# Optimization experiments

Measured on AMD Instinct MI355X. Metric: run time of the kernel, lower is better.

Reference implementation:

```python
import jax, jax.numpy as jnp
import numpy as np

N = 8192   # instances in bag
L = 384    # feature dim (dino_bloom_small -> self.L = 384)
D = 128    # attention hidden dim (self.D)
C = 5      # class_count


def setup_inputs() -> dict:
    key = jax.random.key(0)
    ks = jax.random.split(key, 9)
    s = 0.05
    return {
        "x": jax.random.normal(ks[0], (N, L), dtype=jnp.float32),
        # attention_multi_column: Linear(L,D) -> Tanh -> Linear(D,C)
        "aW1": jax.random.normal(ks[1], (L, D), dtype=jnp.float32) * s,
        "ab1": jax.random.normal(ks[2], (D,), dtype=jnp.float32) * s,
        "aW2": jax.random.normal(ks[3], (D, C), dtype=jnp.float32) * s,
        "ab2": jax.random.normal(ks[4], (C,), dtype=jnp.float32) * s,
        # per-class classifiers: Linear(L,64) -> ReLU -> Linear(64,1), batched over C
        "cW1": jax.random.normal(ks[5], (C, L, 64), dtype=jnp.float32) * s,
        "cb1": jax.random.normal(ks[6], (C, 64), dtype=jnp.float32) * s,
        "cW2": jax.random.normal(ks[7], (C, 64), dtype=jnp.float32) * s,
        "cb2": jax.random.normal(ks[8], (C,), dtype=jnp.float32) * s,
    }


def _pairwise_euclidean(ft):
    # ||a-b|| via Gram expansion; avoids the O(N^2*L) broadcast intermediate
    sq = jnp.sum(ft * ft, axis=1)                      # [N]
    d2 = sq[:, None] + sq[None, :] - 2.0 * (ft @ ft.T)  # [N,N]
    d2 = jnp.maximum(d2, 0.0)
    # safe sqrt (zero on diagonal, matches torch.norm subgradient convention)
    return jnp.where(d2 > 0.0, jnp.sqrt(jnp.where(d2 > 0.0, d2, 1.0)), 0.0)


def reference(x, aW1, ab1, aW2, ab2, cW1, cb1, cW2, cb2):
    ft = x  # encoder is identity for dino_bloom_small
    dist = _pairwise_euclidean(ft)                      # [N,N]
    # multicolumn attention: logits per class, softmax over instances
    att = jnp.tanh(ft @ aW1 + ab1) @ aW2 + ab2          # [N,C]
    att_sm = jax.nn.softmax(att, axis=0)                # softmax over N per class
    bag = att_sm.T @ ft                                 # [C,L] bag features per class
    # per-class classifier heads, batched over class dim
    h = jax.nn.relu(jnp.einsum('cl,clh->ch', bag, cW1) + cb1)  # [C,64]
    pred = jnp.sum(h * cW2, axis=1) + cb2               # [C]
    return pred[None, :], dist
```

## Files before the change

kernel.cpp:

```cpp
#include <hip/hip_runtime.h>
#include <cstdint>
#include <cstddef>

#define N_INST 8192
#define L_DIM  384
#define D_DIM  128
#define C_CLS  5

typedef __bf16 bf16x8 __attribute__((ext_vector_type(8)));
typedef float  f32x4  __attribute__((ext_vector_type(4)));
typedef float  f32x4u __attribute__((ext_vector_type(4), aligned(4)));

typedef __attribute__((address_space(1))) void gvoid_t;
typedef __attribute__((address_space(3))) void lvoid_t;

__device__ __forceinline__ unsigned short f2bf(float f) {
  unsigned u = __float_as_uint(f);
  unsigned r = (u + 0x7FFFu + ((u >> 16) & 1u)) >> 16;
  return (unsigned short)r;
}
__device__ __forceinline__ float bf2f(unsigned short b) {
  return __uint_as_float(((unsigned)b) << 16);
}

__device__ __forceinline__ void gload_lds16(const void* g, void* lds) {
  __builtin_amdgcn_global_load_lds(
      (gvoid_t*)(uintptr_t)g,
      (lvoid_t*)(uint32_t)(uintptr_t)lds,
      16, 0, 0);
}

__global__ __launch_bounds__(256) void prep_x_kernel(
    const float* __restrict__ x, unsigned short* __restrict__ xbf,
    float* __restrict__ sq) {
  int w = threadIdx.x >> 6, lane = threadIdx.x & 63;
  int row = blockIdx.x * 4 + w;
  const float* xr = x + (size_t)row * L_DIM;
  unsigned short* br = xbf + (size_t)row * L_DIM;
  float s = 0.f;
#pragma unroll
  for (int k = 0; k < 6; ++k) {
    float v = xr[lane + 64 * k];
    unsigned short b = f2bf(v);
    br[lane + 64 * k] = b;
    float vb = bf2f(b);
    s = fmaf(vb, vb, s);
  }
#pragma unroll
  for (int off = 32; off; off >>= 1) s += __shfl_down(s, off, 64);
  if (lane == 0) sq[row] = s;
}

__global__ __launch_bounds__(256) void prep_w_kernel(
    const float* __restrict__ aW1, unsigned short* __restrict__ w1t) {
  int idx = blockIdx.x * 256 + threadIdx.x;
  int d = idx / L_DIM, l = idx - d * L_DIM;
  w1t[idx] = f2bf(aW1[(size_t)l * D_DIM + d]);
}

__global__ __launch_bounds__(256, 2) void attn_gemm_kernel(
    const unsigned short* __restrict__ amat,
    const unsigned short* __restrict__ bmat,
    const float* __restrict__ bias,
    const float* __restrict__ aW2,
    const float* __restrict__ ab2,
    float* __restrict__ exp_att,
    float* __restrict__ colsum) {
  __shared__ alignas(16) unsigned short As[128][64];
  __shared__ alignas(16) unsigned short Bs[128][64];
  __shared__ float aW2_l[D_DIM * C_CLS];
  __shared__ float part[128][8][C_CLS];
  __shared__ float cs_l[C_CLS];

  int tid = threadIdx.x;
  int w = tid >> 6, lane = tid & 63;
  int wr = w >> 1, wc = w & 1;
  int i0 = blockIdx.x * 128;

  for (int idx = tid; idx < D_DIM * C_CLS; idx += 256) aW2_l[idx] = aW2[idx];
  if (tid < C_CLS) cs_l[tid] = 0.f;

  const unsigned short* asrc = amat + (size_t)i0 * L_DIM;
  const unsigned short* bsrc = bmat;

  f32x4 acc[4][4];
#pragma unroll
  for (int m = 0; m < 4; ++m)
#pragma unroll
    for (int n = 0; n < 4; ++n) acc[m][n] = (f32x4){0.f, 0.f, 0.f, 0.f};

  int lrow = lane & 15, lkb = lane >> 4;

  for (int kc = 0; kc < 6; ++kc) {
    int k0 = kc * 64;
#pragma unroll
    for (int c = 0; c < 4; ++c) {
      int rb = c * 32 + w * 8;
      gload_lds16(asrc + (size_t)(rb + (lane >> 3)) * L_DIM + k0 + (lane & 7) * 8,
                  &As[rb][0]);
      gload_lds16(bsrc + (size_t)(rb + (lane >> 3)) * L_DIM + k0 + (lane & 7) * 8,
                  &Bs[rb][0]);
    }
    __syncthreads();
#pragma unroll
    for (int kk = 0; kk < 64; kk += 32) {
      bf16x8 af[4], bfr[4];
#pragma unroll
      for (int m = 0; m < 4; ++m)
        af[m] = *(const bf16x8*)&As[wr * 64 + m * 16 + lrow][kk + lkb * 8];
#pragma unroll
      for (int n = 0; n < 4; ++n)
        bfr[n] = *(const bf16x8*)&Bs[wc * 64 + n * 16 + lrow][kk + lkb * 8];
#pragma unroll
      for (int m = 0; m < 4; ++m)
#pragma unroll
        for (int n = 0; n < 4; ++n)
          acc[m][n] = __builtin_amdgcn_mfma_f32_16x16x32_bf16(
              bfr[n], af[m], acc[m][n], 0, 0, 0);
    }
    __syncthreads();
  }

  int q = wc * 4 + lkb;
#pragma unroll
  for (int m = 0; m < 4; ++m) {
    int row_l = wr * 64 + m * 16 + lrow;
    float p[C_CLS] = {0.f, 0.f, 0.f, 0.f, 0.f};
#pragma unroll
    for (int n = 0; n < 4; ++n) {
      int d0 = wc * 64 + n * 16 + lkb * 4;
#pragma unroll
      for (int r = 0; r < 4; ++r) {
        float v = tanhf(acc[m][n][r] + bias[d0 + r]);
        const float* wrow = &aW2_l[(d0 + r) * C_CLS];
#pragma unroll
        for (int c = 0; c < C_CLS; ++c) p[c] = fmaf(v, wrow[c], p[c]);
      }
    }
#pragma unroll
    for (int c = 0; c < C_CLS; ++c) part[row_l][q][c] = p[c];
  }
  __syncthreads();

  if (tid < 128) {
    int gi = i0 + tid;
    float a[C_CLS];
#pragma unroll
    for (int c = 0; c < C_CLS; ++c) a[c] = ab2[c];
#pragma unroll
    for (int qq = 0; qq < 8; ++qq)
#pragma unroll
      for (int c = 0; c < C_CLS; ++c) a[c] += part[tid][qq][c];
#pragma unroll
    for (int c = 0; c < C_CLS; ++c) {
      float e = expf(a[c]);
      exp_att[(size_t)gi * C_CLS + c] = e;
      atomicAdd(&cs_l[c], e);
    }
  }
  __syncthreads();
  if (tid < C_CLS) atomicAdd(&colsum[tid], cs_l[tid]);
}

__global__ __launch_bounds__(256) void head_kernel(
    const unsigned short* __restrict__ xbf, const float* __restrict__ sqv,
    float* __restrict__ F) {
  int w = threadIdx.x >> 6, lane = threadIdx.x & 63;
  int i = blockIdx.x * 4 + w;
  float a0 = 0.f, a1 = 0.f, a2 = 0.f;
  if (lane < 48) {
    const unsigned short* xi = xbf + (size_t)i * L_DIM + lane * 8;
    const unsigned short* x0 = xbf + lane * 8;
    const unsigned short* x1 = xbf + L_DIM + lane * 8;
    const unsigned short* x2 = xbf + 2 * L_DIM + lane * 8;
#pragma unroll
    for (int e = 0; e < 8; ++e) {
      float v = bf2f(xi[e]);
      a0 = fmaf(v, bf2f(x0[e]), a0);
      a1 = fmaf(v, bf2f(x1[e]), a1);
      a2 = fmaf(v, bf2f(x2[e]), a2);
    }
  }
#pragma unroll
  for (int off = 32; off; off >>= 1) {
    a0 += __shfl_down(a0, off, 64);
    a1 += __shfl_down(a1, off, 64);
    a2 += __shfl_down(a2, off, 64);
  }
  if (lane == 0) {
    float si = sqv[i];
    float dots[3] = {a0, a1, a2};
#pragma unroll
    for (int j = 0; j < 3; ++j) {
      float d2 = si + sqv[j] - 2.f * dots[j];
      float dv = (d2 > 0.f) ? sqrtf(d2) : 0.f;
      if (i == j) dv = 0.f;
      F[5 + (size_t)i * N_INST + j] = dv;
    }
  }
}

__global__ __launch_bounds__(256, 2) void dist_kernel(
    const unsigned short* __restrict__ xbf, const float* __restrict__ sqv,
    float* __restrict__ F) {
  __shared__ alignas(16) unsigned short As[128][64];
  __shared__ alignas(16) unsigned short Bs[128][64];

  int tid = threadIdx.x;
  int w = tid >> 6, lane = tid & 63;
  int wr = w >> 1, wc = w & 1;

  int b = blockIdx.x;
  int ti = (int)((129.0 - sqrt(129.0 * 129.0 - 8.0 * (double)b)) * 0.5);
  while ((ti + 1) * (129 - (ti + 1)) / 2 <= b) ++ti;
  while (ti * (129 - ti) / 2 > b) --ti;
  int tj = ti + (b - ti * (129 - ti) / 2);
  int i0 = ti * 128, j0 = tj * 128;

  const unsigned short* asrc = xbf + (size_t)i0 * L_DIM;
  const unsigned short* bsrc = xbf + (size_t)j0 * L_DIM;

  f32x4 acc[4][4];
#pragma unroll
  for (int m = 0; m < 4; ++m)
#pragma unroll
    for (int n = 0; n < 4; ++n) acc[m][n] = (f32x4){0.f, 0.f, 0.f, 0.f};

  int lrow = lane & 15, lkb = lane >> 4;
  int schunk = ((lane & 7) ^ (lane >> 3)) * 8;
  int swz = (lane & 7) << 3;

  for (int kc = 0; kc < 6; ++kc) {
    int k0 = kc * 64;
#pragma unroll
    for (int c = 0; c < 4; ++c) {
      int rb = c * 32 + w * 8;
      gload_lds16(asrc + (size_t)(rb + (lane >> 3)) * L_DIM + k0 + schunk,
                  &As[rb][0]);
      gload_lds16(bsrc + (size_t)(rb + (lane >> 3)) * L_DIM + k0 + schunk,
                  &Bs[rb][0]);
    }
    __syncthreads();
#pragma unroll
    for (int kk = 0; kk < 64; kk += 32) {
      bf16x8 af[4], bfr[4];
#pragma unroll
      for (int m = 0; m < 4; ++m)
        af[m] = *(const bf16x8*)&As[wr * 64 + m * 16 + lrow][(kk + lkb * 8) ^ swz];
#pragma unroll
      for (int n = 0; n < 4; ++n)
        bfr[n] = *(const bf16x8*)&Bs[wc * 64 + n * 16 + lrow][(kk + lkb * 8) ^ swz];
#pragma unroll
      for (int m = 0; m < 4; ++m)
#pragma unroll
        for (int n = 0; n < 4; ++n)
          acc[m][n] = __builtin_amdgcn_mfma_f32_16x16x32_bf16(
              bfr[n], af[m], acc[m][n], 0, 0, 0);
    }
    __syncthreads();
  }

  bool mirror = (ti != tj);
#pragma unroll
  for (int m = 0; m < 4; ++m) {
    int gi = i0 + wr * 64 + m * 16 + lrow;
    float si = sqv[gi];
    float* orow = F + 5 + (size_t)gi * N_INST;
#pragma unroll
    for (int n = 0; n < 4; ++n) {
      int gjb = j0 + wc * 64 + n * 16 + lkb * 4;
      f32x4 sj = *(const f32x4*)&sqv[gjb];
      f32x4u o;
#pragma unroll
      for (int r = 0; r < 4; ++r) {
        float d2 = si + sj[r] - 2.f * acc[m][n][r];
        float dv = (d2 > 0.f) ? sqrtf(d2) : 0.f;
        if (gi == gjb + r) dv = 0.f;
        o[r] = dv;
      }
      *(f32x4u*)&orow[gjb] = o;
      if (mirror) {
#pragma unroll
        for (int r = 0; r < 4; ++r)
          F[5 + (size_t)(gjb + r) * N_INST + gi] = o[r];
      }
    }
  }
}

__global__ __launch_bounds__(256) void bag_kernel(
    const float* __restrict__ x, const float* __restrict__ exp_att,
    float* __restrict__ bagU) {
  int t = threadIdx.x;
  int rbase = blockIdx.x * 32;
  float acc0[C_CLS] = {0, 0, 0, 0, 0}, acc1[C_CLS] = {0, 0, 0, 0, 0};
  int l0 = t, l1 = t + 256;
  for (int i = rbase; i < rbase + 32; ++i) {
    const float* xr = x + (size_t)i * L_DIM;
    float e[C_CLS];
#pragma unroll
    for (int c = 0; c < C_CLS; ++c) e[c] = exp_att[(size_t)i * C_CLS + c];
    float x0 = xr[l0];
#pragma unroll
    for (int c = 0; c < C_CLS; ++c) acc0[c] = fmaf(e[c], x0, acc0[c]);
    if (t < 128) {
      float x1 = xr[l1];
#pragma unroll
      for (int c = 0; c < C_CLS; ++c) acc1[c] = fmaf(e[c], x1, acc1[c]);
    }
  }
#pragma unroll
  for (int c = 0; c < C_CLS; ++c) atomicAdd(&bagU[c * L_DIM + l0], acc0[c]);
  if (t < 128)
#pragma unroll
    for (int c = 0; c < C_CLS; ++c) atomicAdd(&bagU[c * L_DIM + l1], acc1[c]);
}

__global__ __launch_bounds__(256) void final_kernel(
    const float* __restrict__ bagU, const float* __restrict__ colsum,
    const float* __restrict__ cW1, const float* __restrict__ cb1,
    const float* __restrict__ cW2, const float* __restrict__ cb2,
    float* __restrict__ out) {
  __shared__ float bag_s[C_CLS * L_DIM];
  __shared__ float h_s[C_CLS * 64];
  int t = threadIdx.x;
  for (int idx = t; idx < C_CLS * L_DIM; idx += 256) {
    int c = idx / L_DIM;
    bag_s[idx] = bagU[idx] / colsum[c];
  }
  __syncthreads();
  for (int idx = t; idx < C_CLS * 64; idx += 256) {
    int c = idx >> 6, hh = idx & 63;
    float acc = cb1[idx];
    for (int l = 0; l < L_DIM; ++l)
      acc = fmaf(bag_s[c * L_DIM + l], cW1[(size_t)(c * L_DIM + l) * 64 + hh], acc);
    h_s[idx] = fmaxf(acc, 0.f) * cW2[idx];
  }
  __syncthreads();
  if (t < C_CLS) {
    float p = cb2[t];
    for (int hh = 0; hh < 64; ++hh) p += h_s[t * 64 + hh];
    out[t] = p;
  }
}

extern "C" void kernel_launch(void* const* d_in, const int* in_sizes, int n_in,
                              void* d_out, int out_size, void* d_ws,
                              size_t ws_size, hipStream_t stream) {
  const float* x   = (const float*)d_in[0];
  const float* aW1 = (const float*)d_in[1];
  const float* ab1 = (const float*)d_in[2];
  const float* aW2 = (const float*)d_in[3];
  const float* ab2 = (const float*)d_in[4];
  const float* cW1 = (const float*)d_in[5];
  const float* cb1 = (const float*)d_in[6];
  const float* cW2 = (const float*)d_in[7];
  const float* cb2 = (const float*)d_in[8];
  float* outp = (float*)d_out;

  char* ws = (char*)d_ws;
  unsigned short* xbf = (unsigned short*)(ws);
  unsigned short* w1t = (unsigned short*)(ws + 6291456);
  float* sq           = (float*)(ws + 6389760);
  float* exp_att      = (float*)(ws + 6422528);
  float* colsum       = (float*)(ws + 6586368);
  float* bagU         = (float*)(ws + 6586432);

  hipMemsetAsync(ws + 6586368, 0, 64 + C_CLS * L_DIM * 4, stream);

  prep_x_kernel<<<2048, 256, 0, stream>>>(x, xbf, sq);
  prep_w_kernel<<<192, 256, 0, stream>>>(aW1, w1t);
  attn_gemm_kernel<<<64, 256, 0, stream>>>(xbf, w1t, ab1, aW2, ab2, exp_att,
                                           colsum);
  bag_kernel<<<256, 256, 0, stream>>>(x, exp_att, bagU);
  final_kernel<<<1, 256, 0, stream>>>(bagU, colsum, cW1, cb1, cW2, cb2, outp);
  head_kernel<<<2048, 256, 0, stream>>>(xbf, sq, outp);
  dist_kernel<<<2080, 256, 0, stream>>>(xbf, sq, outp);
}
```

Baseline: 210.2 us.

## Compute full distance matrix with aligned column offset instead of symmetric mirroring

The distance kernel stops computing only upper-triangle tiles and mirroring them with scattered transposed stores. It now computes all 64x64 tiles, with columns shifted by 27 so that row stores land on 16-byte aligned addresses given the 5-float output offset. The head kernel is rewritten as an MFMA tile that fills the first 27 columns of every row. This removes strided uncoalesced mirror writes at the cost of roughly doubling the GEMM work.

After: 186.7 us. 11.2% less time.

```diff
diff --git a/kernel.cpp b/kernel.cpp
--- a/kernel.cpp
+++ b/kernel.cpp
@@ -165,37 +165,52 @@
 __global__ __launch_bounds__(256) void head_kernel(
     const unsigned short* __restrict__ xbf, const float* __restrict__ sqv,
     float* __restrict__ F) {
-  int w = threadIdx.x >> 6, lane = threadIdx.x & 63;
-  int i = blockIdx.x * 4 + w;
-  float a0 = 0.f, a1 = 0.f, a2 = 0.f;
-  if (lane < 48) {
-    const unsigned short* xi = xbf + (size_t)i * L_DIM + lane * 8;
-    const unsigned short* x0 = xbf + lane * 8;
-    const unsigned short* x1 = xbf + L_DIM + lane * 8;
-    const unsigned short* x2 = xbf + 2 * L_DIM + lane * 8;
-#pragma unroll
-    for (int e = 0; e < 8; ++e) {
-      float v = bf2f(xi[e]);
-      a0 = fmaf(v, bf2f(x0[e]), a0);
-      a1 = fmaf(v, bf2f(x1[e]), a1);
-      a2 = fmaf(v, bf2f(x2[e]), a2);
-    }
-  }
-#pragma unroll
-  for (int off = 32; off; off >>= 1) {
-    a0 += __shfl_down(a0, off, 64);
-    a1 += __shfl_down(a1, off, 64);
-    a2 += __shfl_down(a2, off, 64);
-  }
-  if (lane == 0) {
-    float si = sqv[i];
-    float dots[3] = {a0, a1, a2};
-#pragma unroll
-    for (int j = 0; j < 3; ++j) {
-      float d2 = si + sqv[j] - 2.f * dots[j];
-      float dv = (d2 > 0.f) ? sqrtf(d2) : 0.f;
-      if (i == j) dv = 0.f;
-      F[5 + (size_t)i * N_INST + j] = dv;
+  int tid = threadIdx.x;
+  int w = tid >> 6, lane = tid & 63;
+  int lrow = lane & 15, lkb = lane >> 4;
+  int rowb = blockIdx.x * 128 + w * 32;
+
+  f32x4 acc[2][2];
+#pragma unroll
+  for (int m = 0; m < 2; ++m)
+#pragma unroll
+    for (int n = 0; n < 2; ++n) acc[m][n] = (f32x4){0.f, 0.f, 0.f, 0.f};
+
+  for (int t = 0; t < 12; ++t) {
+    bf16x8 af[2], bfr[2];
+#pragma unroll
+    for (int m = 0; m < 2; ++m)
+      af[m] = *(const bf16x8*)(xbf + (size_t)(rowb + m * 16 + lrow) * L_DIM +
+                               t * 32 + lkb * 8);
+#pragma unroll
+    for (int n = 0; n < 2; ++n)
+      bfr[n] = *(const bf16x8*)(xbf + (size_t)(n * 16 + lrow) * L_DIM +
+                                t * 32 + lkb * 8);
+#pragma unroll
+    for (int m = 0; m < 2; ++m)
+#pragma unroll
+      for (int n = 0; n < 2; ++n)
+        acc[m][n] = __builtin_amdgcn_mfma_f32_16x16x32_bf16(
+            bfr[n], af[m], acc[m][n], 0, 0, 0);
+  }
+
+#pragma unroll
+  for (int m = 0; m < 2; ++m) {
+    int gi = rowb + m * 16 + lrow;
+    float si = sqv[gi];
+    float* orow = F + 5 + (size_t)gi * N_INST;
+#pragma unroll
+    for (int n = 0; n < 2; ++n) {
+#pragma unroll
+      for (int r = 0; r < 4; ++r) {
+        int j = n * 16 + lkb * 4 + r;
+        if (j < 27) {
+          float d2 = si + sqv[j] - 2.f * acc[m][n][r];
+          float dv = (d2 > 0.f) ? sqrtf(d2) : 0.f;
+          if (gi == j) dv = 0.f;
+          orow[j] = dv;
+        }
+      }
     }
   }
 }
@@ -211,14 +226,12 @@
   int wr = w >> 1, wc = w & 1;
 
   int b = blockIdx.x;
-  int ti = (int)((129.0 - sqrt(129.0 * 129.0 - 8.0 * (double)b)) * 0.5);
-  while ((ti + 1) * (129 - (ti + 1)) / 2 <= b) ++ti;
-  while (ti * (129 - ti) / 2 > b) --ti;
-  int tj = ti + (b - ti * (129 - ti) / 2);
-  int i0 = ti * 128, j0 = tj * 128;
+  int ti = b >> 6, tj = b & 63;
+  int i0 = ti * 128;
+  int jbase = tj * 128 + 27;
 
   const unsigned short* asrc = xbf + (size_t)i0 * L_DIM;
-  const unsigned short* bsrc = xbf + (size_t)j0 * L_DIM;
+  const unsigned short* bsrc = xbf + (size_t)jbase * L_DIM;
 
   f32x4 acc[4][4];
 #pragma unroll
@@ -260,7 +273,6 @@
     __syncthreads();
   }
 
-  bool mirror = (ti != tj);
 #pragma unroll
   for (int m = 0; m < 4; ++m) {
     int gi = i0 + wr * 64 + m * 16 + lrow;
@@ -268,9 +280,9 @@
     float* orow = F + 5 + (size_t)gi * N_INST;
 #pragma unroll
     for (int n = 0; n < 4; ++n) {
-      int gjb = j0 + wc * 64 + n * 16 + lkb * 4;
-      f32x4 sj = *(const f32x4*)&sqv[gjb];
-      f32x4u o;
+      int gjb = jbase + wc * 64 + n * 16 + lkb * 4;
+      f32x4u sj = *(const f32x4u*)&sqv[gjb];
+      f32x4 o;
 #pragma unroll
       for (int r = 0; r < 4; ++r) {
         float d2 = si + sj[r] - 2.f * acc[m][n][r];
@@ -278,11 +290,10 @@
         if (gi == gjb + r) dv = 0.f;
         o[r] = dv;
       }
-      *(f32x4u*)&orow[gjb] = o;
-      if (mirror) {
-#pragma unroll
-        for (int r = 0; r < 4; ++r)
-          F[5 + (size_t)(gjb + r) * N_INST + gi] = o[r];
+      if (gjb < N_INST - 4) {
+        *(f32x4*)&orow[gjb] = o;
+      } else if (gjb < N_INST) {
+        orow[N_INST - 1] = o[0];
       }
     }
   }
@@ -374,6 +385,6 @@
                                            colsum);
   bag_kernel<<<256, 256, 0, stream>>>(x, exp_att, bagU);
   final_kernel<<<1, 256, 0, stream>>>(bagU, colsum, cW1, cb1, cW2, cb2, outp);
-  head_kernel<<<2048, 256, 0, stream>>>(xbf, sq, outp);
-  dist_kernel<<<2080, 256, 0, stream>>>(xbf, sq, outp);
-}
+  head_kernel<<<64, 256, 0, stream>>>(xbf, sq, outp);
+  dist_kernel<<<4096, 256, 0, stream>>>(xbf, sq, outp);
+}
```
